# Kernel optimization log

Hardware: AMD Instinct MI355X
Metric: run time of the kernel (lower is better)

## Reference

```python
import jax, jax.numpy as jnp
import numpy as np
from jax import lax

EPS = 1e-5

def setup_inputs() -> dict:
    key = jax.random.key(0)
    ks = jax.random.split(key, 9)
    B, C, O, H, W = 2, 64, 64, 192, 192
    x = jax.random.normal(ks[0], (B, C, H, W), jnp.float32)
    dw_w = jax.random.normal(ks[1], (C, 1, 3, 3), jnp.float32) * (1.0 / 3.0)
    dw_b = jax.random.normal(ks[2], (C,), jnp.float32) * 0.1
    bn_g = jnp.ones((C,), jnp.float32)
    bn_b = jnp.zeros((C,), jnp.float32)
    bn_m = jax.random.normal(ks[3], (C,), jnp.float32) * 0.1
    bn_v = jax.random.uniform(ks[4], (C,), jnp.float32, 0.5, 1.5)
    # small pointwise weights -> moderate offsets (module inits these to 0)
    pw_w = jax.random.normal(ks[5], (27, C), jnp.float32) * 0.05
    pw_b = jax.random.normal(ks[6], (27,), jnp.float32) * 0.05
    dcn_w = jax.random.normal(ks[7], (O, C, 3, 3), jnp.float32) * (1.0 / np.sqrt(C * 9))
    dcn_b = jax.random.normal(ks[8], (O,), jnp.float32) * 0.1
    return {"x": x, "dw_w": dw_w, "dw_b": dw_b, "bn_g": bn_g, "bn_b": bn_b,
            "bn_m": bn_m, "bn_v": bn_v, "pw_w": pw_w, "pw_b": pw_b,
            "dcn_w": dcn_w, "dcn_b": dcn_b}


def _dcnv2_forward(x, dw_w, dw_b, bn_g, bn_b, bn_m, bn_v, pw_w, pw_b, dcn_w, dcn_b):
    B, C, H, W = x.shape
    O = dcn_w.shape[0]
    K = 9  # 3x3 kernel positions

    # --- offset/mask head: depthwise 3x3 conv + BN(eval) + ReLU + 1x1 conv ---
    h = lax.conv_general_dilated(x, dw_w, (1, 1), ((1, 1), (1, 1)),
                                 feature_group_count=C,
                                 dimension_numbers=("NCHW", "OIHW", "NCHW"))
    h = h + dw_b[None, :, None, None]
    h = (h - bn_m[None, :, None, None]) * lax.rsqrt(bn_v + EPS)[None, :, None, None]
    h = h * bn_g[None, :, None, None] + bn_b[None, :, None, None]
    h = jax.nn.relu(h)
    om = jnp.einsum("bchw,oc->bohw", h, pw_w) + pw_b[None, :, None, None]  # [B,27,H,W]

    off = om[:, :18].reshape(B, K, 2, H, W)  # torchvision layout: (dy, dx) per kernel pos
    dy, dx = off[:, :, 0], off[:, :, 1]      # [B,K,H,W]
    mask = jax.nn.sigmoid(om[:, 18:])        # [B,K,H,W]

    # --- deformable sampling positions ---
    kk = jnp.arange(K)
    ry = (kk // 3 - 1).astype(x.dtype)[None, :, None, None]
    rx = (kk % 3 - 1).astype(x.dtype)[None, :, None, None]
    iy = jnp.arange(H, dtype=x.dtype)[None, None, :, None]
    ix = jnp.arange(W, dtype=x.dtype)[None, None, None, :]
    py = iy + ry + dy  # [B,K,H,W]
    px = ix + rx + dx

    y0 = jnp.floor(py)
    x0 = jnp.floor(px)
    wy1 = py - y0
    wx1 = px - x0
    wy0 = 1.0 - wy1
    wx0 = 1.0 - wx1

    x_flat = x.reshape(B, C, H * W)

    def gather(yi, xi):
        # zero-padded gather at integer coords yi, xi [B,K,H,W] -> [B,C,K,H,W]
        valid = (yi >= 0) & (yi < H) & (xi >= 0) & (xi < W)
        yc = jnp.clip(yi, 0, H - 1).astype(jnp.int32)
        xc = jnp.clip(xi, 0, W - 1).astype(jnp.int32)
        idx = (yc * W + xc).reshape(B, 1, K * H * W)
        v = jnp.take_along_axis(x_flat, idx, axis=2).reshape(B, C, K, H, W)
        return v * valid.astype(x.dtype)[:, None]

    val = (gather(y0, x0) * (wy0 * wx0)[:, None]
           + gather(y0, x0 + 1) * (wy0 * wx1)[:, None]
           + gather(y0 + 1, x0) * (wy1 * wx0)[:, None]
           + gather(y0 + 1, x0 + 1) * (wy1 * wx1)[:, None])  # [B,C,K,H,W]

    val = val * mask[:, None]  # DCNv2 modulation
    out = jnp.einsum("bckhw,ock->bohw", val, dcn_w.reshape(O, C, K))
    out = out + dcn_b[None, :, None, None]

    # --- InstanceNorm2d (affine=False) + ReLU ---
    mu = out.mean(axis=(2, 3), keepdims=True)
    var = out.var(axis=(2, 3), keepdims=True)
    out = (out - mu) * lax.rsqrt(var + EPS)
    return jax.nn.relu(out)


def reference(x, dw_w, dw_b, bn_g, bn_b, bn_m, bn_v, pw_w, pw_b, dcn_w, dcn_b):
    return _dcnv2_forward(x, dw_w, dw_b, bn_g, bn_b, bn_m, bn_v, pw_w, pw_b, dcn_w, dcn_b)
```

## Files before the change

kernel.cpp:

```cpp
#include <hip/hip_runtime.h>
#include <hip/hip_fp16.h>
#include <math.h>

#define H_ 192
#define W_ 192
#define HW_ 36864
#define C_ 64
#define O_ 64
#define B_ 2
#define K_ 9
#define EPS_ 1e-5f

typedef __attribute__((ext_vector_type(8))) _Float16 f16x8;
typedef __attribute__((ext_vector_type(4))) float f32x4;

union U16B { uint4 u; __half2 h[4]; };

__device__ __forceinline__ unsigned int pkh(float lo, float hi) {
  return (unsigned int)__half_as_ushort(__float2half(lo)) |
         ((unsigned int)__half_as_ushort(__float2half(hi)) << 16);
}

__global__ __launch_bounds__(256) void k1_dw(const float* __restrict__ x,
                                             const float* __restrict__ dw_w,
                                             const float* __restrict__ dw_b,
                                             const float* __restrict__ bn_g,
                                             const float* __restrict__ bn_b,
                                             const float* __restrict__ bn_m,
                                             const float* __restrict__ bn_v,
                                             float* __restrict__ h) {
  const int plane = blockIdx.y;
  const int c = plane & (C_ - 1);
  const int p = blockIdx.x * 256 + threadIdx.x;
  const int y = p / W_;
  const int xx = p - y * W_;
  const float* xp = x + (size_t)plane * HW_;
  float w[9];
#pragma unroll
  for (int i = 0; i < 9; ++i) w[i] = dw_w[c * 9 + i];
  float s = 0.f;
#pragma unroll
  for (int dy = 0; dy < 3; ++dy) {
    const int yy = y + dy - 1;
    if (yy < 0 || yy >= H_) continue;
#pragma unroll
    for (int dx = 0; dx < 3; ++dx) {
      const int xc = xx + dx - 1;
      if (xc < 0 || xc >= W_) continue;
      s = fmaf(w[dy * 3 + dx], xp[yy * W_ + xc], s);
    }
  }
  const float scale = bn_g[c] * rsqrtf(bn_v[c] + EPS_);
  const float shift = fmaf(dw_b[c] - bn_m[c], scale, bn_b[c]);
  h[(size_t)plane * HW_ + p] = fmaxf(fmaf(s, scale, shift), 0.f);
}

__global__ __launch_bounds__(256) void k1b_t(const float* __restrict__ x,
                                             unsigned short* __restrict__ xR) {
  const int b = blockIdx.y;
  const int p = blockIdx.x * 256 + threadIdx.x;
  const int y = p / W_;
  const int xx = p - y * W_;
  const float* xp = x + (size_t)b * C_ * HW_ + p;
  uint4* dst = (uint4*)xR + (size_t)b * HW_ * 8;
#pragma unroll
  for (int cc = 0; cc < 8; ++cc) {
    uint4 u;
    u.x = pkh(xp[(size_t)(cc * 8 + 0) * HW_], xp[(size_t)(cc * 8 + 1) * HW_]);
    u.y = pkh(xp[(size_t)(cc * 8 + 2) * HW_], xp[(size_t)(cc * 8 + 3) * HW_]);
    u.z = pkh(xp[(size_t)(cc * 8 + 4) * HW_], xp[(size_t)(cc * 8 + 5) * HW_]);
    u.w = pkh(xp[(size_t)(cc * 8 + 6) * HW_], xp[(size_t)(cc * 8 + 7) * HW_]);
    dst[(y * 8 + cc) * W_ + xx] = u;
  }
}

__global__ __launch_bounds__(256) void k2_pw(const float* __restrict__ h,
                                             const float* __restrict__ pw_w,
                                             const float* __restrict__ pw_b,
                                             float4* __restrict__ om4) {
  __shared__ float wl[C_ * 28];
  const int b = blockIdx.y;
  const int p = blockIdx.x * 256 + threadIdx.x;
  for (int i = threadIdx.x; i < C_ * 28; i += 256) {
    const int c = i / 28, j = i - c * 28;
    wl[i] = (j < 27) ? pw_w[j * C_ + c] : 0.f;
  }
  __syncthreads();
  float s[27];
#pragma unroll
  for (int j = 0; j < 27; ++j) s[j] = 0.f;
  const float* hp = h + (size_t)b * C_ * HW_ + p;
  for (int c = 0; c < C_; ++c) {
    const float hv = hp[(size_t)c * HW_];
    float wv[28];
#pragma unroll
    for (int q = 0; q < 7; ++q)
      *(float4*)&wv[q * 4] = *(const float4*)&wl[c * 28 + q * 4];
#pragma unroll
    for (int j = 0; j < 27; ++j) s[j] = fmaf(hv, wv[j], s[j]);
  }
  float4* op = om4 + (size_t)b * 9 * HW_;
#pragma unroll
  for (int k = 0; k < 9; ++k) {
    const float ry = (float)(k / 3 - 1), rx = (float)(k % 3 - 1);
    float4 v;
    v.x = s[2 * k] + pw_b[2 * k] + ry;
    v.y = s[2 * k + 1] + pw_b[2 * k + 1] + rx;
    v.z = 1.f / (1.f + __expf(-(s[18 + k] + pw_b[18 + k])));
    v.w = 0.f;
    op[(size_t)k * HW_ + p] = v;
  }
}

__global__ __launch_bounds__(256) void k0_wt(const float* __restrict__ dcn_w,
                                             unsigned short* __restrict__ wT2) {
  const int i = blockIdx.x * 256 + threadIdx.x;
  const int o = i / (C_ * 9);
  const int rem = i - o * (C_ * 9);
  const int c = rem / 9;
  const int kk = rem - c * 9;
  wT2[((size_t)(kk * O_) + o) * C_ + c] = __half_as_ushort(__float2half(dcn_w[i]));
}

__global__ __launch_bounds__(256, 4) void k3_dcn(const unsigned short* __restrict__ xR,
                                                 const float4* __restrict__ om4,
                                                 const unsigned short* __restrict__ wT2,
                                                 float* __restrict__ pre,
                                                 float* __restrict__ pstats2) {
  __shared__ __align__(16) unsigned short smem[8192];
  unsigned short* wlds = smem;
  unsigned short* vlds = smem + 4096;

  const int tid = threadIdx.x;
  const int t = (blockIdx.x & 7) * 144 + (blockIdx.x >> 3);
  const int b = t / 576;
  const int p0 = (t - b * 576) * 64;
  const uint4* xr = (const uint4*)xR + (size_t)b * HW_ * 8;
  const float4* omb = om4 + (size_t)b * 9 * HW_;

  const int pxi = tid & 63;
  const int cq = tid >> 6;
  const int lr = pxi & 15;
  const int lg = pxi >> 4;
  const int oo0 = cq * 16;

  const int p = p0 + pxi;
  const int y = p / W_;
  const int xx = p - y * W_;

  f32x4 acc[4];
#pragma unroll
  for (int j = 0; j < 4; ++j) acc[j] = (f32x4){0.f, 0.f, 0.f, 0.f};

  for (int k = 0; k < K_; ++k) {
    const uint4* wsrc = (const uint4*)(wT2 + (k << 12));
    const uint4 wv0 = wsrc[tid];
    const uint4 wv1 = wsrc[tid + 256];
    const float4 od = omb[(size_t)k * HW_ + p];
    const float py = (float)y + od.x;
    const float pxf = (float)xx + od.y;
    const float mk = od.z;
    const float y0f = floorf(py), x0f = floorf(pxf);
    const float wy1 = py - y0f, wx1 = pxf - x0f;
    const float wy0 = 1.f - wy1, wx0 = 1.f - wx1;
    const int y0 = (int)y0f, x0i = (int)x0f;
    const int y1 = y0 + 1, x1i = x0i + 1;
    const bool vy0 = (y0 >= 0) & (y0 < H_);
    const bool vy1 = (y1 >= 0) & (y1 < H_);
    const bool vx0 = (x0i >= 0) & (x0i < W_);
    const bool vx1 = (x1i >= 0) & (x1i < W_);
    const int yc0 = min(max(y0, 0), H_ - 1), yc1 = min(max(y1, 0), H_ - 1);
    const int xc0 = min(max(x0i, 0), W_ - 1), xc1 = min(max(x1i, 0), W_ - 1);
    const float g0 = (vy0 & vx0) ? wy0 * wx0 * mk : 0.f;
    const float g1 = (vy0 & vx1) ? wy0 * wx1 * mk : 0.f;
    const float g2 = (vy1 & vx0) ? wy1 * wx0 * mk : 0.f;
    const float g3 = (vy1 & vx1) ? wy1 * wx1 * mk : 0.f;

    const int ry0 = yc0 * (8 * W_), ry1 = yc1 * (8 * W_);
    const int ca = cq * W_, cb = (cq + 4) * W_;
    U16B a0, a1, a2, a3, b0v, b1v, b2v, b3v;
    a0.u = xr[ry0 + ca + xc0];  b0v.u = xr[ry0 + cb + xc0];
    a1.u = xr[ry0 + ca + xc1];  b1v.u = xr[ry0 + cb + xc1];
    a2.u = xr[ry1 + ca + xc0];  b2v.u = xr[ry1 + cb + xc0];
    a3.u = xr[ry1 + ca + xc1];  b3v.u = xr[ry1 + cb + xc1];

    const __half2 g0h = __float2half2_rn(g0);
    const __half2 g1h = __float2half2_rn(g1);
    const __half2 g2h = __float2half2_rn(g2);
    const __half2 g3h = __float2half2_rn(g3);
    U16B va, vb;
    va.u = make_uint4(0, 0, 0, 0);
    vb.u = make_uint4(0, 0, 0, 0);
#pragma unroll
    for (int i = 0; i < 4; ++i) {
      va.h[i] = __hfma2(a0.h[i], g0h, va.h[i]);
      vb.h[i] = __hfma2(b0v.h[i], g0h, vb.h[i]);
      va.h[i] = __hfma2(a1.h[i], g1h, va.h[i]);
      vb.h[i] = __hfma2(b1v.h[i], g1h, vb.h[i]);
      va.h[i] = __hfma2(a2.h[i], g2h, va.h[i]);
      vb.h[i] = __hfma2(b2v.h[i], g2h, vb.h[i]);
      va.h[i] = __hfma2(a3.h[i], g3h, va.h[i]);
      vb.h[i] = __hfma2(b3v.h[i], g3h, vb.h[i]);
    }

    __syncthreads();
    {
      const int r0 = tid >> 3, b0i = tid & 7;
      ((uint4*)wlds)[(r0 << 3) + (b0i ^ (r0 & 7))] = wv0;
      const int r1 = (tid + 256) >> 3;
      ((uint4*)wlds)[(r1 << 3) + (b0i ^ (r1 & 7))] = wv1;
    }
    {
      const int rsw = pxi & 7;
      ((uint4*)vlds)[(pxi << 3) + (cq ^ rsw)] = va.u;
      ((uint4*)vlds)[(pxi << 3) + ((cq + 4) ^ rsw)] = vb.u;
    }
    __syncthreads();
#pragma unroll
    for (int ks = 0; ks < 2; ++ks) {
      const int kb = (ks << 2) + lg;
      const int ra = oo0 + lr;
      const f16x8 afr = *(const f16x8*)&((const uint4*)wlds)[(ra << 3) + (kb ^ (ra & 7))];
#pragma unroll
      for (int j = 0; j < 4; ++j) {
        const int rb = (j << 4) + lr;
        const f16x8 bfr = *(const f16x8*)&((const uint4*)vlds)[(rb << 3) + (kb ^ (rb & 7))];
        acc[j] = __builtin_amdgcn_mfma_f32_16x16x32_f16(afr, bfr, acc[j], 0, 0, 0);
      }
    }
  }

#pragma unroll
  for (int q = 0; q < 4; ++q) {
    float s = acc[0][q] + acc[1][q] + acc[2][q] + acc[3][q];
    float s2 = fmaf(acc[0][q], acc[0][q],
               fmaf(acc[1][q], acc[1][q],
               fmaf(acc[2][q], acc[2][q], acc[3][q] * acc[3][q])));
#pragma unroll
    for (int m = 1; m < 16; m <<= 1) {
      s += __shfl_xor(s, m);
      s2 += __shfl_xor(s2, m);
    }
    if (lr == 0) {
      const int pll = oo0 + (lg << 2) + q;
      ((float2*)pstats2)[(size_t)t * 64 + pll] = make_float2(s, s2);
    }
  }

  __syncthreads();
  float* fsm = (float*)smem;
#pragma unroll
  for (int j = 0; j < 4; ++j)
#pragma unroll
    for (int q = 0; q < 4; ++q)
      fsm[(oo0 + (lg << 2) + q) * 64 + (j << 4) + lr] = acc[j][q];
  __syncthreads();
  {
    const float4* fsm4 = (const float4*)fsm;
    float* prebase = pre + (size_t)b * O_ * HW_ + p0;
#pragma unroll
    for (int i = 0; i < 4; ++i) {
      const int f = tid + (i << 8);
      const int o = f >> 4;
      const int px4 = (f & 15) << 2;
      *(float4*)&prebase[(size_t)o * HW_ + px4] = fsm4[f];
    }
  }
}

__global__ __launch_bounds__(256) void k4_fin(const float* __restrict__ pstats2,
                                              float* __restrict__ stats) {
  const int pl = blockIdx.x;
  const int b = pl >> 6, o = pl & 63;
  const float2* src = (const float2*)pstats2 + (size_t)b * 576 * 64 + o;
  float s = 0.f, s2 = 0.f;
  for (int tt = threadIdx.x; tt < 576; tt += 256) {
    const float2 v = src[(size_t)tt * 64];
    s += v.x;
    s2 += v.y;
  }
#pragma unroll
  for (int m = 1; m < 64; m <<= 1) {
    s += __shfl_xor(s, m);
    s2 += __shfl_xor(s2, m);
  }
  __shared__ float ls[4], ls2[4];
  const int wid = threadIdx.x >> 6;
  if ((threadIdx.x & 63) == 0) { ls[wid] = s; ls2[wid] = s2; }
  __syncthreads();
  if (threadIdx.x == 0) {
    const float ts = ls[0] + ls[1] + ls[2] + ls[3];
    const float ts2 = ls2[0] + ls2[1] + ls2[2] + ls2[3];
    const float inv = 1.f / (float)HW_;
    const float mu = ts * inv;
    const float var = fmaxf(fmaf(-mu, mu, ts2 * inv), 0.f);
    stats[pl * 2] = mu;
    stats[pl * 2 + 1] = rsqrtf(var + EPS_);
  }
}

__global__ __launch_bounds__(256) void k5_norm(const float* __restrict__ pre,
                                               const float* __restrict__ stats,
                                               float* __restrict__ out) {
  const int i4 = blockIdx.x * 256 + threadIdx.x;
  const int plane = i4 / 9216;
  const float mu = stats[plane * 2];
  const float rs = stats[plane * 2 + 1];
  float4 v = ((const float4*)pre)[i4];
  v.x = fmaxf((v.x - mu) * rs, 0.f);
  v.y = fmaxf((v.y - mu) * rs, 0.f);
  v.z = fmaxf((v.z - mu) * rs, 0.f);
  v.w = fmaxf((v.w - mu) * rs, 0.f);
  ((float4*)out)[i4] = v;
}

extern "C" void kernel_launch(void* const* d_in, const int* in_sizes, int n_in,
                              void* d_out, int out_size, void* d_ws, size_t ws_size,
                              hipStream_t stream) {
  const float* x = (const float*)d_in[0];
  const float* dw_w = (const float*)d_in[1];
  const float* dw_b = (const float*)d_in[2];
  const float* bn_g = (const float*)d_in[3];
  const float* bn_b = (const float*)d_in[4];
  const float* bn_m = (const float*)d_in[5];
  const float* bn_v = (const float*)d_in[6];
  const float* pw_w = (const float*)d_in[7];
  const float* pw_b = (const float*)d_in[8];
  const float* dcn_w = (const float*)d_in[9];
  float* out = (float*)d_out;

  float* ws = (float*)d_ws;
  float* h = ws;
  float4* om4 = (float4*)(h + (size_t)B_ * C_ * HW_);
  unsigned short* wT2 = (unsigned short*)((float*)om4 + (size_t)B_ * 9 * HW_ * 4);
  float* stats = (float*)(wT2 + (size_t)K_ * O_ * C_);
  if (ws_size < (size_t)(4718592 + 2654208 + 18432 + 256) * sizeof(float)) return;
  float* pre = h;
  unsigned short* xR = (unsigned short*)d_out;
  float* pstats2 = (float*)d_out + 2359296;

  k0_wt<<<dim3(144), dim3(256), 0, stream>>>(dcn_w, wT2);
  k1b_t<<<dim3(HW_ / 256, B_), dim3(256), 0, stream>>>(x, xR);
  k1_dw<<<dim3(HW_ / 256, B_ * C_), dim3(256), 0, stream>>>(x, dw_w, dw_b, bn_g, bn_b,
                                                            bn_m, bn_v, h);
  k2_pw<<<dim3(HW_ / 256, B_), dim3(256), 0, stream>>>(h, pw_w, pw_b, om4);
  k3_dcn<<<dim3(B_ * HW_ / 64), dim3(256), 0, stream>>>(xR, om4, wT2, pre, pstats2);
  k4_fin<<<dim3(B_ * O_), dim3(256), 0, stream>>>(pstats2, stats);
  k5_norm<<<dim3(B_ * O_ * HW_ / 4 / 256), dim3(256), 0, stream>>>(pre, stats, out);
}
```

Measured before the change: 102.4 us.

## Fuse depthwise conv with fp16 transpose and store intermediates in fp16

Merges the depthwise conv/BN/ReLU kernel with the x-to-fp16 channel-interleaved transpose, so x is read once and h is written as packed fp16 in the same layout. The pointwise conv now reads fp16 h and uses packed fp16 dot2 instructions. The DCN pre-normalisation output is stored as fp16 and expanded to fp32 in the final normalise kernel. These changes cut memory traffic and launches but lose precision in h and in the pre-norm activations, and k1f uses fewer blocks per launch.

New measurement: 120.3 us. 17.5% more time.

```diff
diff --git a/kernel.cpp b/kernel.cpp
--- a/kernel.cpp
+++ b/kernel.cpp
@@ -12,6 +12,7 @@
 #define EPS_ 1e-5f
 
 typedef __attribute__((ext_vector_type(8))) _Float16 f16x8;
+typedef __attribute__((ext_vector_type(2))) _Float16 f16x2;
 typedef __attribute__((ext_vector_type(4))) float f32x4;
 
 union U16B { uint4 u; __half2 h[4]; };
@@ -21,83 +22,116 @@
          ((unsigned int)__half_as_ushort(__float2half(hi)) << 16);
 }
 
-__global__ __launch_bounds__(256) void k1_dw(const float* __restrict__ x,
-                                             const float* __restrict__ dw_w,
-                                             const float* __restrict__ dw_b,
-                                             const float* __restrict__ bn_g,
-                                             const float* __restrict__ bn_b,
-                                             const float* __restrict__ bn_m,
-                                             const float* __restrict__ bn_v,
-                                             float* __restrict__ h) {
-  const int plane = blockIdx.y;
-  const int c = plane & (C_ - 1);
-  const int p = blockIdx.x * 256 + threadIdx.x;
-  const int y = p / W_;
-  const int xx = p - y * W_;
-  const float* xp = x + (size_t)plane * HW_;
-  float w[9];
-#pragma unroll
-  for (int i = 0; i < 9; ++i) w[i] = dw_w[c * 9 + i];
-  float s = 0.f;
-#pragma unroll
-  for (int dy = 0; dy < 3; ++dy) {
-    const int yy = y + dy - 1;
-    if (yy < 0 || yy >= H_) continue;
-#pragma unroll
-    for (int dx = 0; dx < 3; ++dx) {
-      const int xc = xx + dx - 1;
-      if (xc < 0 || xc >= W_) continue;
-      s = fmaf(w[dy * 3 + dx], xp[yy * W_ + xc], s);
-    }
-  }
-  const float scale = bn_g[c] * rsqrtf(bn_v[c] + EPS_);
-  const float shift = fmaf(dw_b[c] - bn_m[c], scale, bn_b[c]);
-  h[(size_t)plane * HW_ + p] = fmaxf(fmaf(s, scale, shift), 0.f);
-}
-
-__global__ __launch_bounds__(256) void k1b_t(const float* __restrict__ x,
-                                             unsigned short* __restrict__ xR) {
-  const int b = blockIdx.y;
-  const int p = blockIdx.x * 256 + threadIdx.x;
-  const int y = p / W_;
-  const int xx = p - y * W_;
-  const float* xp = x + (size_t)b * C_ * HW_ + p;
-  uint4* dst = (uint4*)xR + (size_t)b * HW_ * 8;
-#pragma unroll
-  for (int cc = 0; cc < 8; ++cc) {
-    uint4 u;
-    u.x = pkh(xp[(size_t)(cc * 8 + 0) * HW_], xp[(size_t)(cc * 8 + 1) * HW_]);
-    u.y = pkh(xp[(size_t)(cc * 8 + 2) * HW_], xp[(size_t)(cc * 8 + 3) * HW_]);
-    u.z = pkh(xp[(size_t)(cc * 8 + 4) * HW_], xp[(size_t)(cc * 8 + 5) * HW_]);
-    u.w = pkh(xp[(size_t)(cc * 8 + 6) * HW_], xp[(size_t)(cc * 8 + 7) * HW_]);
-    dst[(y * 8 + cc) * W_ + xx] = u;
-  }
-}
-
-__global__ __launch_bounds__(256) void k2_pw(const float* __restrict__ h,
+__device__ __forceinline__ float fdot2f(unsigned int a, unsigned int b, float c) {
+#if __has_builtin(__builtin_amdgcn_fdot2)
+  union { unsigned int u; f16x2 h; } ua, ub;
+  ua.u = a; ub.u = b;
+  return __builtin_amdgcn_fdot2(ua.h, ub.h, c, false);
+#else
+  const __half2 ha = *(const __half2*)&a, hb = *(const __half2*)&b;
+  const float2 fa = __half22float2(ha), fb = __half22float2(hb);
+  return fmaf(fa.x, fb.x, fmaf(fa.y, fb.y, c));
+#endif
+}
+
+__global__ __launch_bounds__(256) void k1f(const float* __restrict__ x,
+                                           const float* __restrict__ dw_w,
+                                           const float* __restrict__ dw_b,
+                                           const float* __restrict__ bn_g,
+                                           const float* __restrict__ bn_b,
+                                           const float* __restrict__ bn_m,
+                                           const float* __restrict__ bn_v,
+                                           unsigned short* __restrict__ xR,
+                                           unsigned short* __restrict__ hR) {
+  __shared__ float wls[32][12];
+  const int b = blockIdx.y, hf = blockIdx.z;
+  const int tid = threadIdx.x;
+  for (int i = tid; i < 32 * 12; i += 256) {
+    const int cl = i / 12, j = i - cl * 12;
+    const int c = hf * 32 + cl;
+    if (j < 9) {
+      wls[cl][j] = dw_w[c * 9 + j];
+    } else if (j == 9) {
+      wls[cl][9] = bn_g[c] * rsqrtf(bn_v[c] + EPS_);
+    } else if (j == 10) {
+      const float sc = bn_g[c] * rsqrtf(bn_v[c] + EPS_);
+      wls[cl][10] = fmaf(dw_b[c] - bn_m[c], sc, bn_b[c]);
+    }
+  }
+  __syncthreads();
+  const int p = blockIdx.x * 256 + tid;
+  const int y = p / W_, xx = p - y * W_;
+  const int r0 = max(y - 1, 0) * W_, r1 = y * W_, r2 = min(y + 1, H_ - 1) * W_;
+  const int c0 = max(xx - 1, 0), c1 = xx, c2 = min(xx + 1, W_ - 1);
+  const float mt = (y > 0) ? 1.f : 0.f, mb = (y < H_ - 1) ? 1.f : 0.f;
+  const float ml = (xx > 0) ? 1.f : 0.f, mr = (xx < W_ - 1) ? 1.f : 0.f;
+  const float m[9] = {mt * ml, mt, mt * mr, ml, 1.f, mr, mb * ml, mb, mb * mr};
+  const int off[9] = {r0 + c0, r0 + c1, r0 + c2, r1 + c0, r1 + c1,
+                      r1 + c2, r2 + c0, r2 + c1, r2 + c2};
+  const float* xb = x + ((size_t)b * C_ + hf * 32) * HW_;
+  uint4* xdst = (uint4*)xR + (size_t)b * HW_ * 8 + (size_t)(y * 8) * W_ + xx;
+  uint4* hdst = (uint4*)hR + (size_t)b * HW_ * 8 + (size_t)(y * 8) * W_ + xx;
+#pragma unroll
+  for (int cc = 0; cc < 4; ++cc) {
+    unsigned int hx[4], xv[4];
+#pragma unroll
+    for (int pr = 0; pr < 4; ++pr) {
+      float hv[2], xvv[2];
+#pragma unroll
+      for (int e = 0; e < 2; ++e) {
+        const int cl = cc * 8 + pr * 2 + e;
+        const float* pl = xb + (size_t)cl * HW_;
+        float s = 0.f;
+#pragma unroll
+        for (int j = 0; j < 9; ++j)
+          s = fmaf(wls[cl][j] * m[j], pl[off[j]], s);
+        hv[e] = fmaxf(fmaf(s, wls[cl][9], wls[cl][10]), 0.f);
+        xvv[e] = pl[off[4]];
+      }
+      hx[pr] = pkh(hv[0], hv[1]);
+      xv[pr] = pkh(xvv[0], xvv[1]);
+    }
+    const size_t slot = (size_t)(hf * 4 + cc) * W_;
+    xdst[slot] = make_uint4(xv[0], xv[1], xv[2], xv[3]);
+    hdst[slot] = make_uint4(hx[0], hx[1], hx[2], hx[3]);
+  }
+}
+
+__global__ __launch_bounds__(256) void k2_pw(const unsigned short* __restrict__ hR,
                                              const float* __restrict__ pw_w,
                                              const float* __restrict__ pw_b,
                                              float4* __restrict__ om4) {
-  __shared__ float wl[C_ * 28];
+  __shared__ unsigned int wl2[32 * 28];
   const int b = blockIdx.y;
-  const int p = blockIdx.x * 256 + threadIdx.x;
-  for (int i = threadIdx.x; i < C_ * 28; i += 256) {
-    const int c = i / 28, j = i - c * 28;
-    wl[i] = (j < 27) ? pw_w[j * C_ + c] : 0.f;
-  }
-  __syncthreads();
-  float s[27];
-#pragma unroll
-  for (int j = 0; j < 27; ++j) s[j] = 0.f;
-  const float* hp = h + (size_t)b * C_ * HW_ + p;
-  for (int c = 0; c < C_; ++c) {
-    const float hv = hp[(size_t)c * HW_];
-    float wv[28];
-#pragma unroll
-    for (int q = 0; q < 7; ++q)
-      *(float4*)&wv[q * 4] = *(const float4*)&wl[c * 28 + q * 4];
-#pragma unroll
-    for (int j = 0; j < 27; ++j) s[j] = fmaf(hv, wv[j], s[j]);
+  const int tid = threadIdx.x;
+  for (int i = tid; i < 32 * 28; i += 256) {
+    const int c2 = i / 28, j = i - c2 * 28;
+    wl2[i] = (j < 27) ? pkh(pw_w[j * C_ + 2 * c2], pw_w[j * C_ + 2 * c2 + 1]) : 0u;
+  }
+  __syncthreads();
+  const int p = blockIdx.x * 256 + tid;
+  const int y = p / W_, xx = p - y * W_;
+  const uint4* hr = (const uint4*)hR + (size_t)b * HW_ * 8 + (size_t)(y * 8) * W_ + xx;
+  float s[28];
+#pragma unroll
+  for (int j = 0; j < 28; ++j) s[j] = 0.f;
+#pragma unroll
+  for (int cg = 0; cg < 8; ++cg) {
+    const uint4 hv = hr[(size_t)cg * W_];
+    const unsigned int hu[4] = {hv.x, hv.y, hv.z, hv.w};
+#pragma unroll
+    for (int q = 0; q < 4; ++q) {
+      const int c2 = (cg << 2) + q;
+      const uint4* w4 = (const uint4*)&wl2[c2 * 28];
+#pragma unroll
+      for (int t7 = 0; t7 < 7; ++t7) {
+        const uint4 ww = w4[t7];
+        s[t7 * 4 + 0] = fdot2f(hu[q], ww.x, s[t7 * 4 + 0]);
+        s[t7 * 4 + 1] = fdot2f(hu[q], ww.y, s[t7 * 4 + 1]);
+        s[t7 * 4 + 2] = fdot2f(hu[q], ww.z, s[t7 * 4 + 2]);
+        s[t7 * 4 + 3] = fdot2f(hu[q], ww.w, s[t7 * 4 + 3]);
+      }
+    }
   }
   float4* op = om4 + (size_t)b * 9 * HW_;
 #pragma unroll
@@ -125,7 +159,7 @@
 __global__ __launch_bounds__(256, 4) void k3_dcn(const unsigned short* __restrict__ xR,
                                                  const float4* __restrict__ om4,
                                                  const unsigned short* __restrict__ wT2,
-                                                 float* __restrict__ pre,
+                                                 unsigned short* __restrict__ pre16,
                                                  float* __restrict__ pstats2) {
   __shared__ __align__(16) unsigned short smem[8192];
   unsigned short* wlds = smem;
@@ -257,13 +291,17 @@
   __syncthreads();
   {
     const float4* fsm4 = (const float4*)fsm;
-    float* prebase = pre + (size_t)b * O_ * HW_ + p0;
+    unsigned short* prebase = pre16 + (size_t)b * O_ * HW_ + p0;
 #pragma unroll
     for (int i = 0; i < 4; ++i) {
       const int f = tid + (i << 8);
       const int o = f >> 4;
       const int px4 = (f & 15) << 2;
-      *(float4*)&prebase[(size_t)o * HW_ + px4] = fsm4[f];
+      const float4 v = fsm4[f];
+      uint2 pk;
+      pk.x = pkh(v.x, v.y);
+      pk.y = pkh(v.z, v.w);
+      *(uint2*)&prebase[(size_t)o * HW_ + px4] = pk;
     }
   }
 }
@@ -299,18 +337,23 @@
   }
 }
 
-__global__ __launch_bounds__(256) void k5_norm(const float* __restrict__ pre,
+__global__ __launch_bounds__(256) void k5_norm(const unsigned short* __restrict__ pre16,
                                                const float* __restrict__ stats,
                                                float* __restrict__ out) {
   const int i4 = blockIdx.x * 256 + threadIdx.x;
   const int plane = i4 / 9216;
   const float mu = stats[plane * 2];
   const float rs = stats[plane * 2 + 1];
-  float4 v = ((const float4*)pre)[i4];
-  v.x = fmaxf((v.x - mu) * rs, 0.f);
-  v.y = fmaxf((v.y - mu) * rs, 0.f);
-  v.z = fmaxf((v.z - mu) * rs, 0.f);
-  v.w = fmaxf((v.w - mu) * rs, 0.f);
+  const uint2 pk = ((const uint2*)pre16)[i4];
+  const __half2 h0 = *(const __half2*)&pk.x;
+  const __half2 h1 = *(const __half2*)&pk.y;
+  const float2 f0 = __half22float2(h0);
+  const float2 f1 = __half22float2(h1);
+  float4 v;
+  v.x = fmaxf((f0.x - mu) * rs, 0.f);
+  v.y = fmaxf((f0.y - mu) * rs, 0.f);
+  v.z = fmaxf((f1.x - mu) * rs, 0.f);
+  v.w = fmaxf((f1.y - mu) * rs, 0.f);
   ((float4*)out)[i4] = v;
 }
 
@@ -329,22 +372,20 @@
   const float* dcn_w = (const float*)d_in[9];
   float* out = (float*)d_out;
 
-  float* ws = (float*)d_ws;
-  float* h = ws;
-  float4* om4 = (float4*)(h + (size_t)B_ * C_ * HW_);
-  unsigned short* wT2 = (unsigned short*)((float*)om4 + (size_t)B_ * 9 * HW_ * 4);
+  unsigned short* pre16 = (unsigned short*)d_ws;
+  unsigned short* hR = pre16 + (size_t)B_ * O_ * HW_;
+  float4* om4 = (float4*)(hR + (size_t)B_ * HW_ * C_);
+  unsigned short* wT2 = (unsigned short*)(om4 + (size_t)B_ * 9 * HW_);
   float* stats = (float*)(wT2 + (size_t)K_ * O_ * C_);
-  if (ws_size < (size_t)(4718592 + 2654208 + 18432 + 256) * sizeof(float)) return;
-  float* pre = h;
+  if (ws_size < (size_t)(9437184 + 9437184 + 10616832 + 73728 + 1024)) return;
   unsigned short* xR = (unsigned short*)d_out;
   float* pstats2 = (float*)d_out + 2359296;
 
   k0_wt<<<dim3(144), dim3(256), 0, stream>>>(dcn_w, wT2);
-  k1b_t<<<dim3(HW_ / 256, B_), dim3(256), 0, stream>>>(x, xR);
-  k1_dw<<<dim3(HW_ / 256, B_ * C_), dim3(256), 0, stream>>>(x, dw_w, dw_b, bn_g, bn_b,
-                                                            bn_m, bn_v, h);
-  k2_pw<<<dim3(HW_ / 256, B_), dim3(256), 0, stream>>>(h, pw_w, pw_b, om4);
-  k3_dcn<<<dim3(B_ * HW_ / 64), dim3(256), 0, stream>>>(xR, om4, wT2, pre, pstats2);
+  k1f<<<dim3(HW_ / 256, B_, 2), dim3(256), 0, stream>>>(x, dw_w, dw_b, bn_g, bn_b,
+                                                        bn_m, bn_v, xR, hR);
+  k2_pw<<<dim3(HW_ / 256, B_), dim3(256), 0, stream>>>(hR, pw_w, pw_b, om4);
+  k3_dcn<<<dim3(B_ * HW_ / 64), dim3(256), 0, stream>>>(xR, om4, wT2, pre16, pstats2);
   k4_fin<<<dim3(B_ * O_), dim3(256), 0, stream>>>(pstats2, stats);
-  k5_norm<<<dim3(B_ * O_ * HW_ / 4 / 256), dim3(256), 0, stream>>>(pre, stats, out);
-}
+  k5_norm<<<dim3(B_ * O_ * HW_ / 4 / 256), dim3(256), 0, stream>>>(pre16, stats, out);
+}
```
